# Kernel tuning notes

Hardware: AMD Instinct MI355X
Metric: run time of the kernel (lower is better)

The kernel has to match this reference:

```python
import jax, jax.numpy as jnp
import numpy as np
import math

DIM = 2048
N_PHASES = 8
B, L = 4, 4096


def setup_inputs() -> dict:
    key = jax.random.key(0)
    ks = jax.random.split(key, 12)
    s = 0.02
    return {
        "x": jax.random.normal(ks[0], (B, L, DIM), dtype=jnp.float32),
        # weights stored [in, out] (transposed vs torch Linear)
        "Wp": jax.random.normal(ks[1], (DIM, N_PHASES), dtype=jnp.float32) * s,
        "bp": jnp.zeros((N_PHASES,), dtype=jnp.float32),
        "Wa": jax.random.normal(ks[2], (DIM, N_PHASES), dtype=jnp.float32) * s,
        "ba": jnp.zeros((N_PHASES,), dtype=jnp.float32),
        "Wv": jax.random.normal(ks[3], (DIM, DIM), dtype=jnp.float32) * s,
        "bv": jnp.zeros((DIM,), dtype=jnp.float32),
        "ln_g": jnp.ones((DIM,), dtype=jnp.float32),
        "ln_b": jnp.zeros((DIM,), dtype=jnp.float32),
        "Wo": jax.random.normal(ks[4], (DIM, DIM), dtype=jnp.float32) * s,
        "bo": jnp.zeros((DIM,), dtype=jnp.float32),
    }


def _layernorm(h, g, b, eps=1e-5):
    mu = jnp.mean(h, axis=-1, keepdims=True)
    var = jnp.var(h, axis=-1, keepdims=True)
    return (h - mu) * jax.lax.rsqrt(var + eps) * g + b


def reference(x, Wp, bp, Wa, ba, Wv, bv, ln_g, ln_b, Wo, bo):
    Llen = x.shape[1]
    phase = jnp.tanh(x @ Wp + bp) * math.pi          # [B,L,P]
    amp = jax.nn.softplus(x @ Wa + ba) + 0.1         # [B,L,P]
    value = x @ Wv + bv                              # [B,L,D]
    # (value[...,None,:] * cos_p[...,None] * amp[...,None]).sum(-2)
    # == value * sum_p(cos_p * amp)  -- algebraic factorization, same math.
    cr = jnp.sum(jnp.cos(phase) * amp, axis=-1, keepdims=True)  # [B,L,1]
    ci = jnp.sum(jnp.sin(phase) * amp, axis=-1, keepdims=True)  # [B,L,1]
    bound = value * (cr + ci)                        # real+imag combined
    retrieved = jnp.cumsum(bound, axis=1)            # [B,L,D]
    h = _layernorm(retrieved / math.sqrt(Llen), ln_g, ln_b)
    return x + h @ Wo + bo
```

## Files before the change

kernel.cpp:

```cpp
#include <hip/hip_runtime.h>

#define DIM   2048
#define LSEQ  4096
#define BATCH 4
#define NTOK  (BATCH*LSEQ)
#define NCH   16
#define CHL   (LSEQ/NCH)
#define PI_F  3.14159265358979f
#define NT    (DIM/64)

typedef __bf16 bf16x8 __attribute__((ext_vector_type(8)));
typedef float  f32x4  __attribute__((ext_vector_type(4)));
typedef float  f32x8  __attribute__((ext_vector_type(8)));
typedef unsigned short ushort8 __attribute__((ext_vector_type(8)));

__device__ __forceinline__ unsigned short f2bf(float f) {
    unsigned int u = __float_as_uint(f);
    u += 0x7fffu + ((u >> 16) & 1u);
    return (unsigned short)(u >> 16);
}

__device__ __forceinline__ void gload_lds16(const void* g, void* l) {
    __builtin_amdgcn_global_load_lds(
        (const __attribute__((address_space(1))) void*)g,
        (__attribute__((address_space(3))) void*)l, 16, 0, 0);
}

__global__ __launch_bounds__(256) void k_transpose(const float* __restrict__ src,
                                                   unsigned short* __restrict__ dst) {
    __shared__ float tile[32][33];
    int tx = threadIdx.x, ty = threadIdx.y;
    int k0 = blockIdx.y * 32, n0 = blockIdx.x * 32;
#pragma unroll
    for (int r = 0; r < 4; r++)
        tile[ty + r * 8][tx] = src[(size_t)(k0 + ty + r * 8) * DIM + n0 + tx];
    __syncthreads();
#pragma unroll
    for (int r = 0; r < 4; r++)
        dst[(size_t)(n0 + ty + r * 8) * DIM + k0 + tx] = f2bf(tile[tx][ty + r * 8]);
}

__global__ __launch_bounds__(256) void k_prep_wpa(const float* __restrict__ Wp,
                                                  const float* __restrict__ Wa,
                                                  unsigned short* __restrict__ WpaT) {
    int idx = blockIdx.x * 256 + threadIdx.x;
    int p = idx >> 11, k = idx & (DIM - 1);
    float v = (p < 8) ? Wp[(size_t)k * 8 + p] : Wa[(size_t)k * 8 + (p - 8)];
    WpaT[idx] = f2bf(v);
}

__global__ __launch_bounds__(256) void k_sproj_mfma(const float* __restrict__ x,
                                                    const unsigned short* __restrict__ WpaT,
                                                    const float* __restrict__ bp,
                                                    const float* __restrict__ ba,
                                                    float* __restrict__ s,
                                                    unsigned short* __restrict__ xbf) {
    const int t = threadIdx.x;
    const int w = t >> 6, l = t & 63;
    const int r16 = l & 15, q = l >> 4;
    const int rowbase = blockIdx.x * 64 + w * 16;
    const float* xr = x + (size_t)(rowbase + r16) * DIM + q * 8;
    unsigned short* xw = xbf + (size_t)(rowbase + r16) * DIM + q * 8;
    const unsigned short* wrow = WpaT + r16 * DIM + q * 8;

    f32x4 acc = {};
#pragma unroll 8
    for (int ks = 0; ks < 64; ks++) {
        f32x8 xv = *(const f32x8*)(xr + ks * 32);
        ushort8 xo;
#pragma unroll
        for (int j = 0; j < 8; j++) xo[j] = f2bf(xv[j]);
        *(ushort8*)(xw + ks * 32) = xo;
        bf16x8 av = *(const bf16x8*)&xo;
        bf16x8 bv = *(const bf16x8*)(wrow + ks * 32);
        acc = __builtin_amdgcn_mfma_f32_16x16x32_bf16(av, bv, acc, 0, 0, 0);
    }
    const float bpv = bp[r16 & 7], bav = ba[r16 & 7];
#pragma unroll
    for (int j = 0; j < 4; j++) {
        float z = acc[j];
        float zo = __shfl_xor(z, 8);
        float zp = z + bpv, za = zo + bav;
        float ph = tanhf(zp) * PI_F;
        float amp = (za > 20.f ? za : log1pf(expf(za))) + 0.1f;
        float term = (r16 < 8) ? (cosf(ph) + sinf(ph)) * amp : 0.f;
        term += __shfl_xor(term, 1);
        term += __shfl_xor(term, 2);
        term += __shfl_xor(term, 4);
        if (r16 == 0) s[rowbase + q * 4 + j] = term;
    }
}

__device__ __forceinline__ void stage_unit(const unsigned short* __restrict__ src,
                                           unsigned short* dst, int tid) {
    gload_lds16(src,                     dst + tid * 8);
    gload_lds16(src + (size_t)128 * DIM, dst + (tid + 512) * 8);
}

template <int EPI>
__global__ __launch_bounds__(512, 2) void k_gemm256(const unsigned short* __restrict__ A,
                                                    const unsigned short* __restrict__ Bt,
                                                    const float* __restrict__ bias,
                                                    const float* __restrict__ sc,
                                                    const float* __restrict__ resid,
                                                    float* __restrict__ C,
                                                    float* __restrict__ part) {
    __shared__ __align__(16) unsigned short As[2][2][256 * 32];
    __shared__ __align__(16) unsigned short Bs[2][2][256 * 32];
    __shared__ float colsum[2][256];
    const int tid = threadIdx.x;
    const int w = tid >> 6, lane = tid & 63;
    const int wm = w >> 2, wn = w & 3;
    const int r16 = lane & 15, q = lane >> 4;

    int bid = blockIdx.x;
    int wgs = (bid & 7) * 64 + (bid >> 3);
    int tm = wgs >> 3, tn = wgs & 7;
    int brow = tm * 256, bcol = tn * 256;

    const int kq = ((tid & 3) ^ ((tid >> 3) & 3)) * 8;
    const unsigned short* pA = A  + (size_t)(brow + (tid >> 2)) * DIM + kq;
    const unsigned short* pB = Bt + (size_t)(bcol + (tid >> 2)) * DIM + kq;

    const int qs8 = (q ^ ((r16 >> 1) & 3)) * 8;
    const int offA = (wm * 128 + r16) * 32 + qs8;
    const int offB = (wn * 64  + r16) * 32 + qs8;

    f32x4 acc[8][4] = {};

    stage_unit(pA,      &As[0][0][0], tid);
    stage_unit(pB,      &Bs[0][0][0], tid);
    stage_unit(pA + 32, &As[0][1][0], tid);
    stage_unit(pB + 32, &Bs[0][1][0], tid);
    stage_unit(pA + 64, &As[1][0][0], tid);
    asm volatile("s_waitcnt vmcnt(6)" ::: "memory");
    __builtin_amdgcn_s_barrier();

#pragma unroll 2
    for (int t = 0; t < NT; ++t) {
        const int s = t & 1;
        bf16x8 aF[8], bF[4];

#pragma unroll
        for (int i = 0; i < 8; i++) aF[i] = *(const bf16x8*)(&As[s][0][0] + offA + i * 512);
#pragma unroll
        for (int n = 0; n < 4; n++) bF[n] = *(const bf16x8*)(&Bs[s][0][0] + offB + n * 512);
        stage_unit(pB + (t + 1) * 64,      &Bs[s ^ 1][0][0], tid);
        stage_unit(pA + (t + 1) * 64 + 32, &As[s ^ 1][1][0], tid);
        __builtin_amdgcn_s_setprio(1);
#pragma unroll
        for (int i = 0; i < 8; i++)
#pragma unroll
            for (int n = 0; n < 4; n++)
                acc[i][n] = __builtin_amdgcn_mfma_f32_16x16x32_bf16(aF[i], bF[n], acc[i][n], 0, 0, 0);
        __builtin_amdgcn_s_setprio(0);
        asm volatile("s_waitcnt vmcnt(4)" ::: "memory");
        __builtin_amdgcn_s_barrier();

#pragma unroll
        for (int i = 0; i < 8; i++) aF[i] = *(const bf16x8*)(&As[s][1][0] + offA + i * 512);
#pragma unroll
        for (int n = 0; n < 4; n++) bF[n] = *(const bf16x8*)(&Bs[s][1][0] + offB + n * 512);
        stage_unit(pB + (t + 1) * 64 + 32, &Bs[s ^ 1][1][0], tid);
        stage_unit(pA + (t + 2) * 64,      &As[s][0][0], tid);
        __builtin_amdgcn_s_setprio(1);
#pragma unroll
        for (int i = 0; i < 8; i++)
#pragma unroll
            for (int n = 0; n < 4; n++)
                acc[i][n] = __builtin_amdgcn_mfma_f32_16x16x32_bf16(aF[i], bF[n], acc[i][n], 0, 0, 0);
        __builtin_amdgcn_s_setprio(0);
        asm volatile("s_waitcnt vmcnt(4)" ::: "memory");
        __builtin_amdgcn_s_barrier();
    }

    float cs[4] = {0.f, 0.f, 0.f, 0.f};
#pragma unroll
    for (int mf = 0; mf < 8; mf++) {
        int r0 = brow + wm * 128 + mf * 16 + q * 4;
#pragma unroll
        for (int nf = 0; nf < 4; nf++) {
            int c = bcol + wn * 64 + nf * 16 + r16;
            float bc = bias[c];
#pragma unroll
            for (int j = 0; j < 4; j++) {
                int r = r0 + j;
                float v = acc[mf][nf][j] + bc;
                if (EPI == 0) { v *= sc[r]; cs[nf] += v; }
                else          v += resid[(size_t)r * DIM + c];
                C[(size_t)r * DIM + c] = v;
            }
        }
    }
    if (EPI == 0) {
#pragma unroll
        for (int nf = 0; nf < 4; nf++) {
            float v = cs[nf];
            v += __shfl_xor(v, 16);
            v += __shfl_xor(v, 32);
            if (q == 0) colsum[wm][wn * 64 + nf * 16 + r16] = v;
        }
        __syncthreads();
        if (tid < 256)
            part[(size_t)(brow >> 8) * DIM + bcol + tid] = colsum[0][tid] + colsum[1][tid];
    }
}

__global__ __launch_bounds__(256) void k_scan_offsets(float* __restrict__ part) {
    int tid = blockIdx.x * 256 + threadIdx.x;
    int d = tid & (DIM - 1);
    int b = tid >> 11;
    float run = 0.f;
    for (int ch = 0; ch < NCH; ch++) {
        size_t idx = ((size_t)b * NCH + ch) * DIM + d;
        float v = part[idx];
        part[idx] = run;
        run += v;
    }
}

__global__ __launch_bounds__(256) void k_scan_apply(float* __restrict__ bound,
                                                    const float* __restrict__ part) {
    int tid = blockIdx.x * 256 + threadIdx.x;
    int d = tid & (DIM - 1);
    int ch = (tid >> 11) & (NCH - 1);
    int b = tid >> 15;
    float run = part[tid];
    float* p = bound + ((size_t)b * LSEQ + (size_t)ch * CHL) * DIM + d;
    for (int i = 0; i < CHL; i++) { run += p[(size_t)i * DIM]; p[(size_t)i * DIM] = run; }
}

__global__ __launch_bounds__(256) void k_lnorm(const float* __restrict__ ret,
                                               const float* __restrict__ g,
                                               const float* __restrict__ bta,
                                               unsigned short* __restrict__ h) {
    int row = blockIdx.x, t = threadIdx.x;
    const float4* r4 = (const float4*)(ret + (size_t)row * DIM);
    float4 v0 = r4[2 * t], v1 = r4[2 * t + 1];
    const float scl = 1.0f / 64.0f;
    v0.x *= scl; v0.y *= scl; v0.z *= scl; v0.w *= scl;
    v1.x *= scl; v1.y *= scl; v1.z *= scl; v1.w *= scl;
    float sum = v0.x + v0.y + v0.z + v0.w + v1.x + v1.y + v1.z + v1.w;
    float ss  = v0.x*v0.x + v0.y*v0.y + v0.z*v0.z + v0.w*v0.w
              + v1.x*v1.x + v1.y*v1.y + v1.z*v1.z + v1.w*v1.w;
#pragma unroll
    for (int off = 32; off; off >>= 1) { sum += __shfl_down(sum, off); ss += __shfl_down(ss, off); }
    __shared__ float red[4][2];
    __shared__ float mu_s, rstd_s;
    int w = t >> 6, lane = t & 63;
    if (lane == 0) { red[w][0] = sum; red[w][1] = ss; }
    __syncthreads();
    if (t == 0) {
        float S = red[0][0] + red[1][0] + red[2][0] + red[3][0];
        float Q = red[0][1] + red[1][1] + red[2][1] + red[3][1];
        float mu = S / DIM;
        float var = Q / DIM - mu * mu;
        mu_s = mu; rstd_s = rsqrtf(var + 1e-5f);
    }
    __syncthreads();
    float mu = mu_s, rstd = rstd_s;
    f32x8 gv = *(const f32x8*)(g + t * 8);
    f32x8 bv = *(const f32x8*)(bta + t * 8);
    float vv[8] = { v0.x, v0.y, v0.z, v0.w, v1.x, v1.y, v1.z, v1.w };
    ushort8 o;
#pragma unroll
    for (int j = 0; j < 8; j++) o[j] = f2bf((vv[j] - mu) * rstd * gv[j] + bv[j]);
    *(ushort8*)(h + (size_t)row * DIM + t * 8) = o;
}

extern "C" void kernel_launch(void* const* d_in, const int* in_sizes, int n_in,
                              void* d_out, int out_size, void* d_ws, size_t ws_size,
                              hipStream_t stream) {
    const float* x   = (const float*)d_in[0];
    const float* Wp  = (const float*)d_in[1];
    const float* bp  = (const float*)d_in[2];
    const float* Wa  = (const float*)d_in[3];
    const float* ba  = (const float*)d_in[4];
    const float* Wv  = (const float*)d_in[5];
    const float* bv  = (const float*)d_in[6];
    const float* lng = (const float*)d_in[7];
    const float* lnb = (const float*)d_in[8];
    const float* Wo  = (const float*)d_in[9];
    const float* bo  = (const float*)d_in[10];
    float* out = (float*)d_out;

    char* ws = (char*)d_ws;
    unsigned short* x_bf = (unsigned short*)ws; ws += (size_t)NTOK * DIM * 2;
    unsigned short* WvT  = (unsigned short*)ws; ws += (size_t)DIM * DIM * 2;
    unsigned short* WoT  = (unsigned short*)ws; ws += (size_t)DIM * DIM * 2;
    unsigned short* WpaT = (unsigned short*)ws; ws += (size_t)16 * DIM * 2;
    float* svec          = (float*)ws;          ws += (size_t)NTOK * 4;
    float* bound         = (float*)ws;          ws += (size_t)NTOK * DIM * 4;
    float* part          = (float*)ws;          ws += (size_t)BATCH * NCH * DIM * 4;

    dim3 tb(32, 8);
    k_transpose<<<dim3(64, 64), tb, 0, stream>>>(Wv, WvT);
    k_transpose<<<dim3(64, 64), tb, 0, stream>>>(Wo, WoT);
    k_prep_wpa<<<128, 256, 0, stream>>>(Wp, Wa, WpaT);
    k_sproj_mfma<<<NTOK / 64, 256, 0, stream>>>(x, WpaT, bp, ba, svec, x_bf);

    k_gemm256<0><<<512, 512, 0, stream>>>(x_bf, WvT, bv, svec, nullptr, bound, part);

    k_scan_offsets<<<BATCH * DIM / 256, 256, 0, stream>>>(part);
    k_scan_apply<<<BATCH * NCH * DIM / 256, 256, 0, stream>>>(bound, part);

    k_lnorm<<<NTOK, 256, 0, stream>>>(bound, lng, lnb, x_bf);

    k_gemm256<1><<<512, 512, 0, stream>>>(x_bf, WoT, bo, nullptr, x, out, nullptr);
}
```

Baseline: 450.8 us.

## Store GEMM epilogues transposed as vectors, keep bound in bf16, reuse output buffer

Swaps the MFMA operand order so each lane holds four consecutive columns, which lets the epilogues write vectorized 4-wide stores instead of scalar ones. The intermediate bound tensor is stored in bf16 instead of fp32, and the scan writes its fp32 prefix sums into the output buffer, cutting workspace traffic. The residual in the second GEMM is read from the bf16 copy of x rather than fp32 x. This lowers memory traffic but adds bf16 rounding error to both the cumsum input and the residual added to the output.

```diff
diff --git a/kernel.cpp b/kernel.cpp
--- a/kernel.cpp
+++ b/kernel.cpp
@@ -12,12 +12,16 @@
 typedef __bf16 bf16x8 __attribute__((ext_vector_type(8)));
 typedef float  f32x4  __attribute__((ext_vector_type(4)));
 typedef float  f32x8  __attribute__((ext_vector_type(8)));
+typedef unsigned short ushort4_t __attribute__((ext_vector_type(4)));
 typedef unsigned short ushort8 __attribute__((ext_vector_type(8)));
 
 __device__ __forceinline__ unsigned short f2bf(float f) {
     unsigned int u = __float_as_uint(f);
     u += 0x7fffu + ((u >> 16) & 1u);
     return (unsigned short)(u >> 16);
+}
+__device__ __forceinline__ float bf2f(unsigned short u) {
+    return __uint_as_float((unsigned int)u << 16);
 }
 
 __device__ __forceinline__ void gload_lds16(const void* g, void* l) {
@@ -102,8 +106,9 @@
                                                     const unsigned short* __restrict__ Bt,
                                                     const float* __restrict__ bias,
                                                     const float* __restrict__ sc,
-                                                    const float* __restrict__ resid,
+                                                    const unsigned short* __restrict__ residbf,
                                                     float* __restrict__ C,
+                                                    unsigned short* __restrict__ Cbf,
                                                     float* __restrict__ part) {
     __shared__ __align__(16) unsigned short As[2][2][256 * 32];
     __shared__ __align__(16) unsigned short Bs[2][2][256 * 32];
@@ -126,7 +131,7 @@
     const int offA = (wm * 128 + r16) * 32 + qs8;
     const int offB = (wn * 64  + r16) * 32 + qs8;
 
-    f32x4 acc[8][4] = {};
+    f32x4 acc[4][8] = {};
 
     stage_unit(pA,      &As[0][0][0], tid);
     stage_unit(pB,      &Bs[0][0][0], tid);
@@ -149,10 +154,10 @@
         stage_unit(pA + (t + 1) * 64 + 32, &As[s ^ 1][1][0], tid);
         __builtin_amdgcn_s_setprio(1);
 #pragma unroll
-        for (int i = 0; i < 8; i++)
-#pragma unroll
-            for (int n = 0; n < 4; n++)
-                acc[i][n] = __builtin_amdgcn_mfma_f32_16x16x32_bf16(aF[i], bF[n], acc[i][n], 0, 0, 0);
+        for (int n = 0; n < 4; n++)
+#pragma unroll
+            for (int i = 0; i < 8; i++)
+                acc[n][i] = __builtin_amdgcn_mfma_f32_16x16x32_bf16(bF[n], aF[i], acc[n][i], 0, 0, 0);
         __builtin_amdgcn_s_setprio(0);
         asm volatile("s_waitcnt vmcnt(4)" ::: "memory");
         __builtin_amdgcn_s_barrier();
@@ -165,40 +170,63 @@
         stage_unit(pA + (t + 2) * 64,      &As[s][0][0], tid);
         __builtin_amdgcn_s_setprio(1);
 #pragma unroll
-        for (int i = 0; i < 8; i++)
-#pragma unroll
-            for (int n = 0; n < 4; n++)
-                acc[i][n] = __builtin_amdgcn_mfma_f32_16x16x32_bf16(aF[i], bF[n], acc[i][n], 0, 0, 0);
+        for (int n = 0; n < 4; n++)
+#pragma unroll
+            for (int i = 0; i < 8; i++)
+                acc[n][i] = __builtin_amdgcn_mfma_f32_16x16x32_bf16(bF[n], aF[i], acc[n][i], 0, 0, 0);
         __builtin_amdgcn_s_setprio(0);
         asm volatile("s_waitcnt vmcnt(4)" ::: "memory");
         __builtin_amdgcn_s_barrier();
     }
-
-    float cs[4] = {0.f, 0.f, 0.f, 0.f};
-#pragma unroll
-    for (int mf = 0; mf < 8; mf++) {
-        int r0 = brow + wm * 128 + mf * 16 + q * 4;
-#pragma unroll
-        for (int nf = 0; nf < 4; nf++) {
-            int c = bcol + wn * 64 + nf * 16 + r16;
-            float bc = bias[c];
-#pragma unroll
-            for (int j = 0; j < 4; j++) {
-                int r = r0 + j;
-                float v = acc[mf][nf][j] + bc;
-                if (EPI == 0) { v *= sc[r]; cs[nf] += v; }
-                else          v += resid[(size_t)r * DIM + c];
-                C[(size_t)r * DIM + c] = v;
+    asm volatile("s_waitcnt vmcnt(0)" ::: "memory");
+
+    float cs[4][4] = {};
+#pragma unroll
+    for (int nf = 0; nf < 4; nf++) {
+        const int c0 = bcol + wn * 64 + nf * 16 + q * 4;
+        const f32x4 b4 = *(const f32x4*)(bias + c0);
+#pragma unroll
+        for (int mi = 0; mi < 8; mi++) {
+            const int r = brow + wm * 128 + mi * 16 + r16;
+            if (EPI == 0) {
+                const float scr = sc[r];
+                ushort4_t o;
+#pragma unroll
+                for (int j = 0; j < 4; j++) {
+                    float v = (acc[nf][mi][j] + b4[j]) * scr;
+                    cs[nf][j] += v;
+                    o[j] = f2bf(v);
+                }
+                *(ushort4_t*)(Cbf + (size_t)r * DIM + c0) = o;
+            } else {
+                ushort4_t rsd = *(const ushort4_t*)(residbf + (size_t)r * DIM + c0);
+                f32x4 v;
+#pragma unroll
+                for (int j = 0; j < 4; j++) v[j] = acc[nf][mi][j] + b4[j] + bf2f(rsd[j]);
+                *(f32x4*)(C + (size_t)r * DIM + c0) = v;
             }
         }
     }
     if (EPI == 0) {
 #pragma unroll
-        for (int nf = 0; nf < 4; nf++) {
-            float v = cs[nf];
-            v += __shfl_xor(v, 16);
-            v += __shfl_xor(v, 32);
-            if (q == 0) colsum[wm][wn * 64 + nf * 16 + r16] = v;
+        for (int nf = 0; nf < 4; nf++)
+#pragma unroll
+            for (int j = 0; j < 4; j++) {
+                float v = cs[nf][j];
+                v += __shfl_xor(v, 1);
+                v += __shfl_xor(v, 2);
+                v += __shfl_xor(v, 4);
+                v += __shfl_xor(v, 8);
+                cs[nf][j] = v;
+            }
+        if (r16 == 0) {
+#pragma unroll
+            for (int nf = 0; nf < 4; nf++) {
+                f32x4 o;
+#pragma unroll
+                for (int j = 0; j < 4; j++) o[j] = cs[nf][j];
+                *(f32x4*)(&colsum[wm][wn * 64 + nf * 16 + q * 4]) = o;
+            }
         }
         __syncthreads();
         if (tid < 256)
@@ -219,15 +247,21 @@
     }
 }
 
-__global__ __launch_bounds__(256) void k_scan_apply(float* __restrict__ bound,
-                                                    const float* __restrict__ part) {
+__global__ __launch_bounds__(256) void k_scan_apply(const unsigned short* __restrict__ boundbf,
+                                                    const float* __restrict__ part,
+                                                    float* __restrict__ ret) {
     int tid = blockIdx.x * 256 + threadIdx.x;
     int d = tid & (DIM - 1);
     int ch = (tid >> 11) & (NCH - 1);
     int b = tid >> 15;
     float run = part[tid];
-    float* p = bound + ((size_t)b * LSEQ + (size_t)ch * CHL) * DIM + d;
-    for (int i = 0; i < CHL; i++) { run += p[(size_t)i * DIM]; p[(size_t)i * DIM] = run; }
+    size_t base = ((size_t)b * LSEQ + (size_t)ch * CHL) * DIM + d;
+    const unsigned short* p = boundbf + base;
+    float* o = ret + base;
+    for (int i = 0; i < CHL; i++) {
+        run += bf2f(p[(size_t)i * DIM]);
+        o[(size_t)i * DIM] = run;
+    }
 }
 
 __global__ __launch_bounds__(256) void k_lnorm(const float* __restrict__ ret,
@@ -285,13 +319,15 @@
     float* out = (float*)d_out;
 
     char* ws = (char*)d_ws;
-    unsigned short* x_bf = (unsigned short*)ws; ws += (size_t)NTOK * DIM * 2;
-    unsigned short* WvT  = (unsigned short*)ws; ws += (size_t)DIM * DIM * 2;
-    unsigned short* WoT  = (unsigned short*)ws; ws += (size_t)DIM * DIM * 2;
-    unsigned short* WpaT = (unsigned short*)ws; ws += (size_t)16 * DIM * 2;
-    float* svec          = (float*)ws;          ws += (size_t)NTOK * 4;
-    float* bound         = (float*)ws;          ws += (size_t)NTOK * DIM * 4;
-    float* part          = (float*)ws;          ws += (size_t)BATCH * NCH * DIM * 4;
+    unsigned short* x_bf  = (unsigned short*)ws; ws += (size_t)NTOK * DIM * 2;
+    unsigned short* h_bf  = (unsigned short*)ws; ws += (size_t)NTOK * DIM * 2;
+    unsigned short* WvT   = (unsigned short*)ws; ws += (size_t)DIM * DIM * 2;
+    unsigned short* WoT   = (unsigned short*)ws; ws += (size_t)DIM * DIM * 2;
+    unsigned short* WpaT  = (unsigned short*)ws; ws += (size_t)16 * DIM * 2;
+    float* svec           = (float*)ws;          ws += (size_t)NTOK * 4;
+    unsigned short* bound = (unsigned short*)ws; ws += (size_t)NTOK * DIM * 2;
+    float* part           = (float*)ws;          ws += (size_t)BATCH * NCH * DIM * 4;
+    float* ret            = out;
 
     dim3 tb(32, 8);
     k_transpose<<<dim3(64, 64), tb, 0, stream>>>(Wv, WvT);
@@ -299,12 +335,12 @@
     k_prep_wpa<<<128, 256, 0, stream>>>(Wp, Wa, WpaT);
     k_sproj_mfma<<<NTOK / 64, 256, 0, stream>>>(x, WpaT, bp, ba, svec, x_bf);
 
-    k_gemm256<0><<<512, 512, 0, stream>>>(x_bf, WvT, bv, svec, nullptr, bound, part);
+    k_gemm256<0><<<512, 512, 0, stream>>>(x_bf, WvT, bv, svec, nullptr, nullptr, bound, part);
 
     k_scan_offsets<<<BATCH * DIM / 256, 256, 0, stream>>>(part);
-    k_scan_apply<<<BATCH * NCH * DIM / 256, 256, 0, stream>>>(bound, part);
-
-    k_lnorm<<<NTOK, 256, 0, stream>>>(bound, lng, lnb, x_bf);
-
-    k_gemm256<1><<<512, 512, 0, stream>>>(x_bf, WoT, bo, nullptr, x, out, nullptr);
-}
+    k_scan_apply<<<BATCH * NCH * DIM / 256, 256, 0, stream>>>(bound, part, ret);
+
+    k_lnorm<<<NTOK, 256, 0, stream>>>(ret, lng, lnb, h_bf);
+
+    k_gemm256<1><<<512, 512, 0, stream>>>(h_bf, WoT, bo, nullptr, x_bf, out, nullptr, nullptr);
+}
```

Measured after the change: 477.5 us. 5.9% more time.
